# Kernel optimization log

Measured on AMD Instinct MI355X. Metric: run time of the kernel, lower is better.

Reference implementation:

```python
import jax, jax.numpy as jnp
import numpy as np

EPS_NORM = 1e-12   # F.normalize eps
EPS_Q = 1e-5       # quant scale clamp

def simple_rmsnorm(x):
    # F.normalize(x, dim=-1) * sqrt(dim)  ==  x / sqrt(mean(x^2))
    d = x.shape[-1]
    n = jnp.maximum(jnp.linalg.norm(x, axis=-1, keepdims=True), EPS_NORM)
    return x / n * jnp.sqrt(jnp.asarray(d, x.dtype))

def activation_quant(x):
    # per-token 8-bit absmax quant
    scale = 127.0 / jnp.clip(jnp.max(jnp.abs(x), axis=-1, keepdims=True), EPS_Q, None)
    return jnp.clip(jnp.round(x * scale), -128.0, 127.0) / scale

def weight_quant(w):
    # per-tensor ternary quant: scale = 1 / mean|w|
    scale = 1.0 / jnp.clip(jnp.mean(jnp.abs(w)), EPS_Q, None)
    return jnp.clip(jnp.round(w * scale), -1.0, 1.0) / scale

def bitlinear158(x, w):
    xn = simple_rmsnorm(x)
    # straight-through estimators
    xq = xn + jax.lax.stop_gradient(activation_quant(xn) - xn)
    wq = w + jax.lax.stop_gradient(weight_quant(w) - w)
    # w is [out, in] like nn.Linear
    return jnp.einsum('bsd,od->bso', xq, wq)

def setup_inputs() -> dict:
    key = jax.random.key(0)
    k1, k2, k3 = jax.random.split(key, 3)
    dim, inner = 2048, 8192
    x = jax.random.normal(k1, (4, 2048, dim), dtype=jnp.float32)
    w1 = jax.random.normal(k2, (inner, dim), dtype=jnp.float32) * 0.02
    w2 = jax.random.normal(k3, (dim, inner), dtype=jnp.float32) * 0.02
    return {"x": x, "w1": w1, "w2": w2}

def reference(x, w1, w2):
    h = bitlinear158(x, w1)
    h = jax.nn.gelu(h, approximate=False)  # nn.GELU() default = exact erf
    return bitlinear158(h, w2)
```

## Files before the change

kernel.cpp:

```cpp
#include <hip/hip_runtime.h>
#include <hip/hip_bf16.h>
#include <hip/hip_fp16.h>

typedef __attribute__((ext_vector_type(4))) int i32x4;
typedef __attribute__((ext_vector_type(8))) unsigned short u16x8;
typedef __attribute__((ext_vector_type(8))) char c8;
typedef __attribute__((ext_vector_type(4))) char c4;
typedef unsigned int u32;
typedef unsigned short u16;

#define SCH0() __builtin_amdgcn_sched_barrier(0)

__device__ __forceinline__ void gload_lds16(const void* g, void* l) {
  __builtin_amdgcn_global_load_lds((const u32 __attribute__((address_space(1)))*)g,
                                   (u32 __attribute__((address_space(3)))*)l, 16, 0, 0);
}
__device__ __forceinline__ float h2f(u16 u) { return __half2float(__ushort_as_half(u)); }
__device__ __forceinline__ u16  f2h(float f){ return __half_as_ushort(__float2half_rn(f)); }

__global__ __launch_bounds__(256) void quant_x_kernel(const float* __restrict__ x,
    char* __restrict__ qx, float* __restrict__ invs) {
  const int D = 2048;
  int row = blockIdx.x, tid = threadIdx.x;
  const float* xr = x + (size_t)row * D;
  float4 a = ((const float4*)xr)[tid * 2], b = ((const float4*)xr)[tid * 2 + 1];
  float v[8] = {a.x, a.y, a.z, a.w, b.x, b.y, b.z, b.w};
  double ss = 0; float mx = 0.0f;
#pragma unroll
  for (int i = 0; i < 8; i++) { ss += (double)v[i] * v[i]; mx = fmaxf(mx, fabsf(v[i])); }
  __shared__ double sd[256]; __shared__ float sf[256];
  sd[tid] = ss; sf[tid] = mx; __syncthreads();
  for (int o = 128; o > 0; o >>= 1) {
    if (tid < o) { sd[tid] += sd[tid + o]; sf[tid] = fmaxf(sf[tid], sf[tid + o]); }
    __syncthreads();
  }
  __shared__ float bn, bs;
  if (tid == 0) {
    float n = fmaxf((float)sqrt(sd[0]), 1e-12f);
    float amax = sf[0] * (sqrtf((float)D) / n);
    float cl = fmaxf(amax, 1e-5f);
    bn = n; bs = 127.0f / cl;
    invs[row] = cl / 127.0f;
  }
  __syncthreads();
  float n = bn, s = bs, sq = sqrtf((float)D);
  c8 q;
#pragma unroll
  for (int i = 0; i < 8; i++) {
    float xn = (v[i] / n) * sq;
    float r = rintf(xn * s);
    r = fminf(fmaxf(r, -128.0f), 127.0f);
    q[i] = (char)(int)r;
  }
  *(c8*)&qx[(size_t)row * D + tid * 8] = q;
}

__global__ __launch_bounds__(256) void absum_partial(const float* __restrict__ w,
    double* __restrict__ part, int n4) {
  int tid = threadIdx.x;
  double s = 0;
  for (int i = blockIdx.x * 256 + tid; i < n4; i += gridDim.x * 256) {
    float4 v = ((const float4*)w)[i];
    s += (double)fabsf(v.x) + (double)fabsf(v.y) + (double)fabsf(v.z) + (double)fabsf(v.w);
  }
  __shared__ double sd[256];
  sd[tid] = s; __syncthreads();
  for (int o = 128; o > 0; o >>= 1) { if (tid < o) sd[tid] += sd[tid + o]; __syncthreads(); }
  if (tid == 0) part[blockIdx.x] = sd[0];
}

__global__ __launch_bounds__(256) void wscale_final(const double* __restrict__ part,
    float* __restrict__ wsc) {
  int tid = threadIdx.x;
  __shared__ double sd[256];
  sd[tid] = part[tid] + part[tid + 256]; __syncthreads();
  for (int o = 128; o > 0; o >>= 1) { if (tid < o) sd[tid] += sd[tid + o]; __syncthreads(); }
  double s1 = sd[0]; __syncthreads();
  sd[tid] = part[512 + tid] + part[768 + tid]; __syncthreads();
  for (int o = 128; o > 0; o >>= 1) { if (tid < o) sd[tid] += sd[tid + o]; __syncthreads(); }
  if (tid == 0) {
    float m1 = (float)(s1 / 16777216.0);
    float m2 = (float)(sd[0] / 16777216.0);
    float d1 = fmaxf(m1, 1e-5f), d2 = fmaxf(m2, 1e-5f);
    wsc[0] = 1.0f / d1; wsc[1] = d1; wsc[2] = 1.0f / d2; wsc[3] = d2;
  }
}

__global__ __launch_bounds__(256) void quant_w_kernel(const float* __restrict__ w,
    char* __restrict__ q, const float* __restrict__ wsc, int widx, int n4) {
  float s = wsc[widx];
  for (int i = blockIdx.x * 256 + threadIdx.x; i < n4; i += gridDim.x * 256) {
    float4 v = ((const float4*)w)[i];
    c4 o;
    o[0] = (char)(int)(fminf(fmaxf(rintf(v.x * s), -1.0f), 1.0f));
    o[1] = (char)(int)(fminf(fmaxf(rintf(v.y * s), -1.0f), 1.0f));
    o[2] = (char)(int)(fminf(fmaxf(rintf(v.z * s), -1.0f), 1.0f));
    o[3] = (char)(int)(fminf(fmaxf(rintf(v.w * s), -1.0f), 1.0f));
    ((c4*)q)[i] = o;
  }
}

template <int EPI>
__global__ __launch_bounds__(512, 2) void gemm_i8(const char* __restrict__ A,
    const char* __restrict__ B, int N, int K, size_t ldA, size_t ldB, int gridN,
    const float* __restrict__ rowscale, const float* __restrict__ wsc,
    int widx, void* __restrict__ outp) {
  __shared__ __align__(16) char sm[3][2][16384];
  const int tid = threadIdx.x;
  const int lane = tid & 63, w = tid >> 6;
  const int wm = w >> 2, wn = w & 3;
  const int llo = lane & 15, lhi = lane >> 4;
  const int koff = ((lhi ^ ((llo >> 1) & 3)) << 4);

  const int nwg = gridDim.x, cpx = nwg >> 3;
  const int swz = (blockIdx.x & 7) * cpx + (blockIdx.x >> 3);
  const int bm = swz / gridN, bn = swz % gridN;

  const int NT = K >> 6;
  const size_t Abase = (size_t)(bm * 256) * ldA;
  const size_t Bbase = (size_t)(bn * 256) * ldB;

  const int rs = tid >> 2;
  const int kbs = (((tid & 3) ^ ((tid >> 3) & 3)) << 4);

  auto stage = [&](int mat, int buf, int hf, int kt) {
    const char* G = (mat == 0) ? A : B;
    size_t ld = (mat == 0) ? ldA : ldB;
    size_t base = (mat == 0) ? Abase : Bbase;
    gload_lds16(G + base + (size_t)(hf * 128 + rs) * ld + (size_t)kt * 64 + kbs,
                &sm[buf][mat][hf * 8192 + tid * 16]);
  };
  auto stage_tile = [&](int buf, int kt) {
    stage(0, buf, 0, kt); stage(1, buf, 0, kt);
    stage(0, buf, 1, kt); stage(1, buf, 1, kt);
  };

  i32x4 alo[4], ahi[4], blo[2], bhi[2];
  auto readA = [&](int buf, int half, i32x4 (&dst)[4]) {
    int rbase = wm * 128 + half * 64 + llo;
#pragma unroll
    for (int f = 0; f < 4; f++)
      dst[f] = *(const i32x4*)&sm[buf][0][(rbase + f * 16) * 64 + koff];
  };
  auto readB = [&](int buf, int half, i32x4 (&dst)[2]) {
    int rbase = wn * 64 + half * 32 + llo;
#pragma unroll
    for (int f = 0; f < 2; f++)
      dst[f] = *(const i32x4*)&sm[buf][1][(rbase + f * 16) * 64 + koff];
  };

  i32x4 acc[8][4];
#pragma unroll
  for (int m = 0; m < 8; m++)
#pragma unroll
    for (int n = 0; n < 4; n++) acc[m][n] = (i32x4){0, 0, 0, 0};

  auto mmaq = [&](i32x4 (&av)[4], i32x4 (&bv)[2], int mh, int nh) {
    __builtin_amdgcn_s_setprio(1);
#pragma unroll
    for (int m = 0; m < 4; m++)
#pragma unroll
      for (int n = 0; n < 2; n++)
        acc[mh * 4 + m][nh * 2 + n] =
            __builtin_amdgcn_mfma_i32_16x16x64_i8(av[m], bv[n],
                                                  acc[mh * 4 + m][nh * 2 + n], 0, 0, 0);
    __builtin_amdgcn_s_setprio(0);
  };

  stage_tile(0, 0);
  asm volatile("s_nop 0" ::: "memory");
  stage_tile(1, 1);
  asm volatile("s_waitcnt vmcnt(4)\n\ts_barrier" ::: "memory");
  readA(0, 0, alo); readB(0, 0, blo);

  int bR = 0, bN = 1, bS = 2;
  for (int t = 0; t < NT; t++) {
    if (t + 2 < NT) stage_tile(bS, t + 2);
    SCH0();
    readB(bR, 1, bhi);
    SCH0();
    mmaq(alo, blo, 0, 0);
    SCH0();
    readA(bR, 1, ahi);
    SCH0();
    mmaq(alo, bhi, 0, 1);
    mmaq(ahi, blo, 1, 0);
    SCH0();
    if (t + 1 < NT) {
      if (t + 2 < NT) asm volatile("s_waitcnt vmcnt(4) lgkmcnt(0)\n\ts_barrier" ::: "memory");
      else            asm volatile("s_waitcnt vmcnt(0) lgkmcnt(0)\n\ts_barrier" ::: "memory");
      readA(bN, 0, alo); readB(bN, 0, blo);
      SCH0();
    }
    mmaq(ahi, bhi, 1, 1);
    int tmp = bR; bR = bN; bN = bS; bS = tmp;
  }

  float wdeq = wsc[widx];
#pragma unroll
  for (int mf = 0; mf < 8; mf++) {
#pragma unroll
    for (int reg = 0; reg < 4; reg++) {
      int r = bm * 256 + wm * 128 + mf * 16 + lhi * 4 + reg;
      float deq = rowscale[r] * wdeq;
#pragma unroll
      for (int nf = 0; nf < 4; nf++) {
        int c = bn * 256 + wn * 64 + nf * 16 + llo;
        float val = (float)acc[mf][nf][reg] * deq;
        if (EPI == 0) {
          float g = 0.5f * val * (1.0f + erff(val * 0.70710678118654752440f));
          ((u16*)outp)[(size_t)r * N + c] = f2h(g);
        } else {
          ((float*)outp)[(size_t)r * N + c] = val;
        }
      }
    }
  }
}

__global__ __launch_bounds__(256) void quant_h_kernel(u16* __restrict__ h, float* __restrict__ invs) {
  const int D = 8192;
  int row = blockIdx.x, tid = threadIdx.x;
  u16* hr = h + (size_t)row * D;
  float v[32];
#pragma unroll
  for (int j = 0; j < 4; j++) {
    u16x8 u = *(const u16x8*)&hr[j * 2048 + tid * 8];
#pragma unroll
    for (int e = 0; e < 8; e++) v[j * 8 + e] = h2f(u[e]);
  }
  double ss = 0; float mx = 0.0f;
#pragma unroll
  for (int i = 0; i < 32; i++) { ss += (double)v[i] * v[i]; mx = fmaxf(mx, fabsf(v[i])); }
  __shared__ double sd[256]; __shared__ float sf[256];
  sd[tid] = ss; sf[tid] = mx; __syncthreads();
  for (int o = 128; o > 0; o >>= 1) {
    if (tid < o) { sd[tid] += sd[tid + o]; sf[tid] = fmaxf(sf[tid], sf[tid + o]); }
    __syncthreads();
  }
  __shared__ float bn, bs;
  if (tid == 0) {
    float n = fmaxf((float)sqrt(sd[0]), 1e-12f);
    float amax = sf[0] * (sqrtf((float)D) / n);
    float cl = fmaxf(amax, 1e-5f);
    bn = n; bs = 127.0f / cl;
    invs[row] = cl / 127.0f;
  }
  __syncthreads();
  float n = bn, s = bs, sq = sqrtf((float)D);
  char* hq = (char*)hr;
#pragma unroll
  for (int j = 0; j < 4; j++) {
    c8 q;
#pragma unroll
    for (int e = 0; e < 8; e++) {
      float xn = (v[j * 8 + e] / n) * sq;
      float r = rintf(xn * s);
      r = fminf(fmaxf(r, -128.0f), 127.0f);
      q[e] = (char)(int)r;
    }
    *(c8*)&hq[j * 2048 + tid * 8] = q;
  }
}

extern "C" void kernel_launch(void* const* d_in, const int* in_sizes, int n_in,
                              void* d_out, int out_size, void* d_ws, size_t ws_size,
                              hipStream_t stream) {
  const float* x  = (const float*)d_in[0];
  const float* w1 = (const float*)d_in[1];
  const float* w2 = (const float*)d_in[2];

  char* ws = (char*)d_ws;
  char*   qx     = (char*)(ws + 0);
  char*   w1q    = (char*)(ws + 16777216);
  char*   w2q    = (char*)(ws + 33554432);
  u16*    h      = (u16*)(ws + 50331648);
  float*  invs_x = (float*)(ws + 184549376);
  float*  invs_h = (float*)(ws + 184582144);
  double* part   = (double*)(ws + 184614912);
  float*  wsc    = (float*)(ws + 184623104);

  quant_x_kernel<<<8192, 256, 0, stream>>>(x, qx, invs_x);
  absum_partial<<<512, 256, 0, stream>>>(w1, part, 4194304);
  absum_partial<<<512, 256, 0, stream>>>(w2, part + 512, 4194304);
  wscale_final<<<1, 256, 0, stream>>>(part, wsc);
  quant_w_kernel<<<2048, 256, 0, stream>>>(w1, w1q, wsc, 0, 4194304);
  quant_w_kernel<<<2048, 256, 0, stream>>>(w2, w2q, wsc, 2, 4194304);
  gemm_i8<0><<<1024, 512, 0, stream>>>(qx, w1q, 8192, 2048, 2048, 2048, 32,
                                       invs_x, wsc, 1, (void*)h);
  quant_h_kernel<<<8192, 256, 0, stream>>>(h, invs_h);
  gemm_i8<1><<<256, 512, 0, stream>>>((const char*)h, w2q, 2048, 8192, 16384, 8192, 8,
                                      invs_h, wsc, 3, d_out);
}
```

Baseline: 452.5 us.

## Merge prep kernels into fewer launches and band-swizzle GEMM tile order

Merges the x-quantization kernel and the two weight abs-sum kernels into one launch using block-index ranges. It also merges the two weight-quantization launches into one. The GEMM tile mapping changes to bands of four M-tiles walked along N, so tiles that share B data run close together for better L2 reuse. This cuts launch overhead and the serialized small-kernel tails, at the cost of branchy kernels. The GEMM order change could help or hurt cache locality.

```diff
diff --git a/kernel.cpp b/kernel.cpp
--- a/kernel.cpp
+++ b/kernel.cpp
@@ -18,55 +18,60 @@
 __device__ __forceinline__ float h2f(u16 u) { return __half2float(__ushort_as_half(u)); }
 __device__ __forceinline__ u16  f2h(float f){ return __half_as_ushort(__float2half_rn(f)); }
 
-__global__ __launch_bounds__(256) void quant_x_kernel(const float* __restrict__ x,
-    char* __restrict__ qx, float* __restrict__ invs) {
-  const int D = 2048;
-  int row = blockIdx.x, tid = threadIdx.x;
-  const float* xr = x + (size_t)row * D;
-  float4 a = ((const float4*)xr)[tid * 2], b = ((const float4*)xr)[tid * 2 + 1];
-  float v[8] = {a.x, a.y, a.z, a.w, b.x, b.y, b.z, b.w};
-  double ss = 0; float mx = 0.0f;
-#pragma unroll
-  for (int i = 0; i < 8; i++) { ss += (double)v[i] * v[i]; mx = fmaxf(mx, fabsf(v[i])); }
-  __shared__ double sd[256]; __shared__ float sf[256];
-  sd[tid] = ss; sf[tid] = mx; __syncthreads();
-  for (int o = 128; o > 0; o >>= 1) {
-    if (tid < o) { sd[tid] += sd[tid + o]; sf[tid] = fmaxf(sf[tid], sf[tid + o]); }
+__global__ __launch_bounds__(256) void prep_kernel(const float* __restrict__ x,
+    char* __restrict__ qx, float* __restrict__ invs,
+    const float* __restrict__ w1, const float* __restrict__ w2,
+    double* __restrict__ part) {
+  const int tid = threadIdx.x;
+  __shared__ double sd[256];
+  __shared__ float sf[256];
+  if (blockIdx.x < 8192) {
+    const int D = 2048;
+    int row = blockIdx.x;
+    const float* xr = x + (size_t)row * D;
+    float4 a = ((const float4*)xr)[tid * 2], b = ((const float4*)xr)[tid * 2 + 1];
+    float v[8] = {a.x, a.y, a.z, a.w, b.x, b.y, b.z, b.w};
+    double ss = 0; float mx = 0.0f;
+#pragma unroll
+    for (int i = 0; i < 8; i++) { ss += (double)v[i] * v[i]; mx = fmaxf(mx, fabsf(v[i])); }
+    sd[tid] = ss; sf[tid] = mx; __syncthreads();
+    for (int o = 128; o > 0; o >>= 1) {
+      if (tid < o) { sd[tid] += sd[tid + o]; sf[tid] = fmaxf(sf[tid], sf[tid + o]); }
+      __syncthreads();
+    }
+    __shared__ float bn, bs;
+    if (tid == 0) {
+      float n = fmaxf((float)sqrt(sd[0]), 1e-12f);
+      float amax = sf[0] * (sqrtf((float)D) / n);
+      float cl = fmaxf(amax, 1e-5f);
+      bn = n; bs = 127.0f / cl;
+      invs[row] = cl / 127.0f;
+    }
     __syncthreads();
-  }
-  __shared__ float bn, bs;
-  if (tid == 0) {
-    float n = fmaxf((float)sqrt(sd[0]), 1e-12f);
-    float amax = sf[0] * (sqrtf((float)D) / n);
-    float cl = fmaxf(amax, 1e-5f);
-    bn = n; bs = 127.0f / cl;
-    invs[row] = cl / 127.0f;
-  }
-  __syncthreads();
-  float n = bn, s = bs, sq = sqrtf((float)D);
-  c8 q;
-#pragma unroll
-  for (int i = 0; i < 8; i++) {
-    float xn = (v[i] / n) * sq;
-    float r = rintf(xn * s);
-    r = fminf(fmaxf(r, -128.0f), 127.0f);
-    q[i] = (char)(int)r;
-  }
-  *(c8*)&qx[(size_t)row * D + tid * 8] = q;
-}
-
-__global__ __launch_bounds__(256) void absum_partial(const float* __restrict__ w,
-    double* __restrict__ part, int n4) {
-  int tid = threadIdx.x;
-  double s = 0;
-  for (int i = blockIdx.x * 256 + tid; i < n4; i += gridDim.x * 256) {
-    float4 v = ((const float4*)w)[i];
-    s += (double)fabsf(v.x) + (double)fabsf(v.y) + (double)fabsf(v.z) + (double)fabsf(v.w);
-  }
-  __shared__ double sd[256];
-  sd[tid] = s; __syncthreads();
-  for (int o = 128; o > 0; o >>= 1) { if (tid < o) sd[tid] += sd[tid + o]; __syncthreads(); }
-  if (tid == 0) part[blockIdx.x] = sd[0];
+    float n = bn, s = bs, sq = sqrtf((float)D);
+    c8 q;
+#pragma unroll
+    for (int i = 0; i < 8; i++) {
+      float xn = (v[i] / n) * sq;
+      float r = rintf(xn * s);
+      r = fminf(fmaxf(r, -128.0f), 127.0f);
+      q[i] = (char)(int)r;
+    }
+    *(c8*)&qx[(size_t)row * D + tid * 8] = q;
+  } else {
+    const int n4 = 4194304;
+    const bool isw2 = blockIdx.x >= 8704;
+    const float* w = isw2 ? w2 : w1;
+    const int vb = blockIdx.x - (isw2 ? 8704 : 8192);
+    double s = 0;
+    for (int i = vb * 256 + tid; i < n4; i += 512 * 256) {
+      float4 v = ((const float4*)w)[i];
+      s += (double)fabsf(v.x) + (double)fabsf(v.y) + (double)fabsf(v.z) + (double)fabsf(v.w);
+    }
+    sd[tid] = s; __syncthreads();
+    for (int o = 128; o > 0; o >>= 1) { if (tid < o) sd[tid] += sd[tid + o]; __syncthreads(); }
+    if (tid == 0) part[(isw2 ? 512 : 0) + vb] = sd[0];
+  }
 }
 
 __global__ __launch_bounds__(256) void wscale_final(const double* __restrict__ part,
@@ -86,10 +91,16 @@
   }
 }
 
-__global__ __launch_bounds__(256) void quant_w_kernel(const float* __restrict__ w,
-    char* __restrict__ q, const float* __restrict__ wsc, int widx, int n4) {
-  float s = wsc[widx];
-  for (int i = blockIdx.x * 256 + threadIdx.x; i < n4; i += gridDim.x * 256) {
+__global__ __launch_bounds__(256) void quant_w_kernel(const float* __restrict__ w1,
+    char* __restrict__ q1, const float* __restrict__ w2, char* __restrict__ q2,
+    const float* __restrict__ wsc) {
+  const int n4 = 4194304;
+  const bool isw2 = blockIdx.x >= 2048;
+  const float* w = isw2 ? w2 : w1;
+  char* q = isw2 ? q2 : q1;
+  float s = isw2 ? wsc[2] : wsc[0];
+  const int vb = blockIdx.x - (isw2 ? 2048 : 0);
+  for (int i = vb * 256 + threadIdx.x; i < n4; i += 2048 * 256) {
     float4 v = ((const float4*)w)[i];
     c4 o;
     o[0] = (char)(int)(fminf(fmaxf(rintf(v.x * s), -1.0f), 1.0f));
@@ -114,7 +125,9 @@
 
   const int nwg = gridDim.x, cpx = nwg >> 3;
   const int swz = (blockIdx.x & 7) * cpx + (blockIdx.x >> 3);
-  const int bm = swz / gridN, bn = swz % gridN;
+  const int band = gridN << 2;
+  const int g = swz / band, idx = swz % band;
+  const int bm = (g << 2) + (idx & 3), bn = idx >> 2;
 
   const int NT = K >> 6;
   const size_t Abase = (size_t)(bm * 256) * ldA;
@@ -280,12 +293,9 @@
   double* part   = (double*)(ws + 184614912);
   float*  wsc    = (float*)(ws + 184623104);
 
-  quant_x_kernel<<<8192, 256, 0, stream>>>(x, qx, invs_x);
-  absum_partial<<<512, 256, 0, stream>>>(w1, part, 4194304);
-  absum_partial<<<512, 256, 0, stream>>>(w2, part + 512, 4194304);
+  prep_kernel<<<9216, 256, 0, stream>>>(x, qx, invs_x, w1, w2, part);
   wscale_final<<<1, 256, 0, stream>>>(part, wsc);
-  quant_w_kernel<<<2048, 256, 0, stream>>>(w1, w1q, wsc, 0, 4194304);
-  quant_w_kernel<<<2048, 256, 0, stream>>>(w2, w2q, wsc, 2, 4194304);
+  quant_w_kernel<<<4096, 256, 0, stream>>>(w1, w1q, w2, w2q, wsc);
   gemm_i8<0><<<1024, 512, 0, stream>>>(qx, w1q, 8192, 2048, 2048, 2048, 32,
                                        invs_x, wsc, 1, (void*)h);
   quant_h_kernel<<<8192, 256, 0, stream>>>(h, invs_h);
```

Result: faster. 427.6 us (-5.5%).
